# Kernel optimization log

Measured on AMD Instinct MI355X. Metric: run time of the kernel, lower is better.

The kernel has to match this reference:

```python
import jax, jax.numpy as jnp
import numpy as np
from jax import lax

B, N, S = 4, 16384, 4096
D1, D2 = 128, 256
MLP = (256, 128)
EPS_W = 1e-8
EPS_BN = 1e-5
BIG = 1e8


def setup_inputs() -> dict:
    key = jax.random.key(0)
    ks = jax.random.split(key, 10)
    inp = {
        "xyz1": jax.random.normal(ks[0], (B, 3, N), jnp.float32),
        "xyz2": jax.random.normal(ks[1], (B, 3, S), jnp.float32),
        "points1": jax.random.normal(ks[2], (B, D1, N), jnp.float32),
        "points2": jax.random.normal(ks[3], (B, D2, S), jnp.float32),
        "idx1": jnp.repeat(jnp.arange(B, dtype=jnp.int32), N).reshape(B, N),
        "idx2": jnp.repeat(jnp.arange(B, dtype=jnp.int32), S).reshape(B, S),
    }
    cin = D1 + D2
    inp["w1"] = jax.random.normal(ks[4], (MLP[0], cin), jnp.float32) * 0.05
    inp["b1"] = jnp.zeros((MLP[0],), jnp.float32)
    inp["g1"] = jnp.ones((MLP[0],), jnp.float32)
    inp["be1"] = jnp.zeros((MLP[0],), jnp.float32)
    inp["w2"] = jax.random.normal(ks[5], (MLP[1], MLP[0]), jnp.float32) * 0.05
    inp["b2"] = jnp.zeros((MLP[1],), jnp.float32)
    inp["g2"] = jnp.ones((MLP[1],), jnp.float32)
    inp["be2"] = jnp.zeros((MLP[1],), jnp.float32)
    return inp


def _bn_relu(x, gamma, beta):
    # training-mode batchnorm over (B, N) per channel, then relu; x: [B, C, N]
    mean = jnp.mean(x, axis=(0, 2), keepdims=True)
    var = jnp.var(x, axis=(0, 2), keepdims=True)  # biased, as torch BN
    xn = (x - mean) * lax.rsqrt(var + EPS_BN)
    return jax.nn.relu(xn * gamma[None, :, None] + beta[None, :, None])


def _fp_forward(xyz1, xyz2, points1, points2, idx1, idx2,
                w1, b1, g1, be1, w2, b2, g2, be2):
    x1 = jnp.transpose(xyz1, (0, 2, 1))  # [B, N, 3]
    x2 = jnp.transpose(xyz2, (0, 2, 1))  # [B, S, 3]
    p2 = jnp.transpose(points2, (0, 2, 1))  # [B, S, D2]

    # squared pairwise distances [B, N, S]
    d = -2.0 * jnp.einsum('bnc,bsc->bns', x1, x2)
    d = d + jnp.sum(x1 * x1, -1)[:, :, None] + jnp.sum(x2 * x2, -1)[:, None, :]
    d = jnp.where(idx1[:, :, None] == idx2[:, None, :], d, jnp.inf)

    # 3 nearest neighbors (top-k on negated distances == sort-ascending take 3)
    neg_d3, idx3 = lax.top_k(-d, 3)          # [B, N, 3]
    d3 = -neg_d3
    recip = 1.0 / (d3 + EPS_W)
    weight = recip / jnp.sum(recip, axis=2, keepdims=True)
    weight = jnp.where(d3 > BIG, 0.0, weight)
    weight = jnp.nan_to_num(weight)

    gathered = jax.vmap(lambda p, i: p[i])(p2, idx3)   # [B, N, 3, D2]
    interp = jnp.sum(gathered * weight[..., None], axis=2)  # [B, N, D2]

    newp = jnp.concatenate([jnp.transpose(points1, (0, 2, 1)), interp], axis=-1)
    newp = jnp.transpose(newp, (0, 2, 1))  # [B, D1+D2, N]

    # 1x1 conv -> BN -> relu, twice
    h = jnp.einsum('bcn,oc->bon', newp, w1) + b1[None, :, None]
    h = _bn_relu(h, g1, be1)
    h = jnp.einsum('bcn,oc->bon', h, w2) + b2[None, :, None]
    h = _bn_relu(h, g2, be2)
    return h


def reference(xyz1, xyz2, points1, points2, idx1, idx2,
              w1, b1, g1, be1, w2, b2, g2, be2):
    return _fp_forward(xyz1, xyz2, points1, points2, idx1, idx2,
                       w1, b1, g1, be1, w2, b2, g2, be2)
```

## Files before the change

kernel.cpp:

```cpp
#include <hip/hip_runtime.h>
#include <hip/hip_bf16.h>

#define INF_F (__builtin_inff())

typedef __attribute__((ext_vector_type(8))) short bf16x8;
typedef __attribute__((ext_vector_type(4))) float f32x4;

__device__ __forceinline__ unsigned short f2bf(float f) {
  __hip_bfloat16 h = __float2bfloat16(f);
  return __builtin_bit_cast(unsigned short, h);
}
__device__ __forceinline__ float bf2f(unsigned short u) {
  return __uint_as_float((unsigned)u << 16);
}


__global__ __launch_bounds__(256) void transpose_k(const float* __restrict__ in,
                                                   float* __restrict__ out) {
  __shared__ float tile[32][33];
  int b = blockIdx.z;
  int s0 = blockIdx.x * 32;
  int k0 = blockIdx.y * 32;
  int tx = threadIdx.x, ty = threadIdx.y;
  const float* src = in + ((size_t)b * 256 + k0) * 4096 + s0;
  for (int r = ty; r < 32; r += 8) tile[r][tx] = src[(size_t)r * 4096 + tx];
  __syncthreads();
  float* dst = out + ((size_t)b * 4096 + s0) * 256 + k0;
  for (int r = ty; r < 32; r += 8) dst[(size_t)r * 256 + tx] = tile[tx][r];
}

__global__ __launch_bounds__(256) void p1t_k(const float* __restrict__ p1,
                                             unsigned short* __restrict__ X) {
  __shared__ float tile[32][33];
  int b = blockIdx.z;
  int n0 = blockIdx.x * 32;
  int c0 = blockIdx.y * 32;
  int tx = threadIdx.x, ty = threadIdx.y;
  const float* src = p1 + ((size_t)b * 128 + c0) * 16384 + n0;
  for (int r = ty; r < 32; r += 8) tile[r][tx] = src[(size_t)r * 16384 + tx];
  __syncthreads();
  for (int r = ty; r < 32; r += 8)
    X[((size_t)(b * 16384 + n0 + r)) * 384 + c0 + tx] = f2bf(tile[tx][r]);
}

__global__ __launch_bounds__(256) void wcvt_k(const float* __restrict__ w1,
                                              const float* __restrict__ w2,
                                              unsigned short* __restrict__ w1b,
                                              unsigned short* __restrict__ w2b) {
  int id = blockIdx.x * 256 + threadIdx.x;
  if (id < 98304) w1b[id] = f2bf(w1[id]);
  else w2b[id - 98304] = f2bf(w2[id - 98304]);
}

__global__ __launch_bounds__(256) void knn_k(const float* __restrict__ xyz1,
                                             const float* __restrict__ xyz2,
                                             const int* __restrict__ idx1,
                                             const int* __restrict__ idx2,
                                             float* __restrict__ rec) {
  __shared__ float4 sP[2048];
  int bid = blockIdx.x;
  int nchunk = bid >> 1, shalf = bid & 1;
  int b = nchunk >> 7;
  int n0 = (nchunk & 127) * 128;
  int t = threadIdx.x;
  int q = t & 127, sp = t >> 7;
  int n = n0 + q;
  int common = idx1[b * 16384 + n0];
  int sbase = shalf << 11;
  for (int s = t; s < 2048; s += 256) {
    int gs = sbase + s;
    float x = xyz2[(b * 3 + 0) * 4096 + gs];
    float y = xyz2[(b * 3 + 1) * 4096 + gs];
    float z = xyz2[(b * 3 + 2) * 4096 + gs];
    float w = fmaf(x, x, fmaf(y, y, z * z));
    int sid = idx2[b * 4096 + gs];
    w = (sid == common) ? w : 3e38f;
    sP[s] = make_float4(x, y, z, w);
  }
  __syncthreads();
  float px = xyz1[(b * 3 + 0) * 16384 + n];
  float py = xyz1[(b * 3 + 1) * 16384 + n];
  float pz = xyz1[(b * 3 + 2) * 16384 + n];
  int myid = idx1[b * 16384 + n];
  float pn = fmaf(px, px, fmaf(py, py, pz * pz));
  float e0 = INF_F, e1 = INF_F, e2 = INF_F;
  int j0 = 0, j1 = 0, j2 = 0;
  int sBeg = sp << 10, sEnd = sBeg + 1024;
#pragma unroll 4
  for (int s = sBeg; s < sEnd; ++s) {
    float4 p = sP[s];
    float dot = fmaf(px, p.x, fmaf(py, p.y, pz * p.z));
    float d = fmaf(-2.f, dot, pn + p.w);
    if (d < e2) {
      int sj = sbase + s;
      bool l0 = d < e0, l1 = d < e1;
      e2 = l1 ? e1 : d;
      j2 = l1 ? j1 : sj;
      e1 = l0 ? e0 : (l1 ? d : e1);
      j1 = l0 ? j0 : (l1 ? sj : j1);
      e0 = l0 ? d : e0;
      j0 = l0 ? sj : j0;
    }
  }
  if (__builtin_expect(myid != common, 0)) {
    e0 = e1 = e2 = INF_F; j0 = j1 = j2 = 0;
    for (int s = sBeg; s < sEnd; ++s) {
      int gs = sbase + s;
      float x = xyz2[(b * 3 + 0) * 4096 + gs];
      float y = xyz2[(b * 3 + 1) * 4096 + gs];
      float z = xyz2[(b * 3 + 2) * 4096 + gs];
      float w = fmaf(x, x, fmaf(y, y, z * z));
      float dot = fmaf(px, x, fmaf(py, y, pz * z));
      float d = fmaf(-2.f, dot, pn + w);
      d = (idx2[b * 4096 + gs] == myid) ? d : INF_F;
      if (d < e2) {
        bool l0 = d < e0, l1 = d < e1;
        e2 = l1 ? e1 : d; j2 = l1 ? j1 : gs;
        e1 = l0 ? e0 : (l1 ? d : e1); j1 = l0 ? j0 : (l1 ? gs : j1);
        e0 = l0 ? d : e0; j0 = l0 ? gs : j0;
      }
    }
  }
  __syncthreads();
  float* sf = (float*)sP;
  int* si = (int*)sP;
  if (sp == 1) {
    sf[0 * 128 + q] = e0; sf[1 * 128 + q] = e1; sf[2 * 128 + q] = e2;
    si[3 * 128 + q] = j0; si[4 * 128 + q] = j1; si[5 * 128 + q] = j2;
  }
  __syncthreads();
  if (t < 128) {
#pragma unroll
    for (int w = 0; w < 3; ++w) {
      float d = sf[w * 128 + t];
      int sj = si[(w + 3) * 128 + t];
      bool l0 = (d < e0) || (d == e0 && sj < j0);
      bool l1 = (d < e1) || (d == e1 && sj < j1);
      bool l2 = (d < e2) || (d == e2 && sj < j2);
      e2 = l1 ? e1 : (l2 ? d : e2);
      j2 = l1 ? j1 : (l2 ? sj : j2);
      e1 = l0 ? e0 : (l1 ? d : e1);
      j1 = l0 ? j0 : (l1 ? sj : j1);
      e0 = l0 ? d : e0;
      j0 = l0 ? sj : j0;
    }
    float* r = &rec[(((size_t)nchunk * 128 + t) * 2 + shalf) * 6];
    r[0] = e0; r[1] = e1; r[2] = e2;
    ((int*)r)[3] = j0; ((int*)r)[4] = j1; ((int*)r)[5] = j2;
  }
}

__global__ __launch_bounds__(256) void knnmerge_k(const float* __restrict__ rec,
                                                  int* __restrict__ idx3,
                                                  float* __restrict__ wgt) {
  int i = blockIdx.x * 256 + threadIdx.x;
  const float* rA = &rec[(size_t)i * 12];
  const int* iA = (const int*)rA;
  float e0 = rA[0], e1 = rA[1], e2 = rA[2];
  int j0 = iA[3], j1 = iA[4], j2 = iA[5];
#pragma unroll
  for (int w = 0; w < 3; ++w) {
    float d = rA[6 + w];
    int sj = iA[9 + w];
    bool l0 = (d < e0) || (d == e0 && sj < j0);
    bool l1 = (d < e1) || (d == e1 && sj < j1);
    bool l2 = (d < e2) || (d == e2 && sj < j2);
    e2 = l1 ? e1 : (l2 ? d : e2);
    j2 = l1 ? j1 : (l2 ? sj : j2);
    e1 = l0 ? e0 : (l1 ? d : e1);
    j1 = l0 ? j0 : (l1 ? sj : j1);
    e0 = l0 ? d : e0;
    j0 = l0 ? sj : j0;
  }
  float r0 = 1.f / (e0 + 1e-8f);
  float r1 = 1.f / (e1 + 1e-8f);
  float r2 = 1.f / (e2 + 1e-8f);
  float rs = r0 + r1 + r2;
  float w0 = (e0 > 1e8f) ? 0.f : r0 / rs;
  float w1 = (e1 > 1e8f) ? 0.f : r1 / rs;
  float w2 = (e2 > 1e8f) ? 0.f : r2 / rs;
  idx3[(size_t)i * 3 + 0] = j0; idx3[(size_t)i * 3 + 1] = j1; idx3[(size_t)i * 3 + 2] = j2;
  wgt[(size_t)i * 3 + 0] = w0;  wgt[(size_t)i * 3 + 1] = w1;  wgt[(size_t)i * 3 + 2] = w2;
}

__global__ __launch_bounds__(256) void interp_k(const float* __restrict__ p2t,
                                                const int* __restrict__ idx3,
                                                const float* __restrict__ wgt,
                                                unsigned short* __restrict__ X) {
  int i0 = blockIdx.x * 128;
  int b = i0 >> 14;
  int k = threadIdx.x;
  const float* base = p2t + (size_t)b * 4096 * 256;
#pragma unroll 2
  for (int ii = 0; ii < 128; ++ii) {
    int i = i0 + ii;
    int id0 = idx3[i * 3 + 0], id1 = idx3[i * 3 + 1], id2 = idx3[i * 3 + 2];
    float w0 = wgt[i * 3 + 0], w1v = wgt[i * 3 + 1], w2v = wgt[i * 3 + 2];
    float v = w0 * base[id0 * 256 + k];
    v = fmaf(w1v, base[id1 * 256 + k], v);
    v = fmaf(w2v, base[id2 * 256 + k], v);
    X[(size_t)i * 384 + 128 + k] = f2bf(v);
  }
}

__global__ __launch_bounds__(256) void gemm1_k(const unsigned short* __restrict__ X,
                                               const unsigned short* __restrict__ Wb,
                                               unsigned short* __restrict__ h1T) {
  __shared__ unsigned short sW[128][40];
  __shared__ unsigned short sX[128][40];
  int t = threadIdx.x;
  int i0 = blockIdx.x * 128;
  int c0 = blockIdx.y * 128;
  int w = t >> 6, lane = t & 63;
  int wc = (w & 1) * 64, wn = (w >> 1) * 64;
  int l15 = lane & 15, g = lane >> 4;
  f32x4 acc[4][4];
#pragma unroll
  for (int a = 0; a < 4; ++a)
#pragma unroll
    for (int bq = 0; bq < 4; ++bq) acc[a][bq] = (f32x4)0.f;
  int sr = t & 127, sh = t >> 7;
  for (int kc = 0; kc < 12; ++kc) {
    int k0 = kc * 32;
    __syncthreads();
    {
      const uint4* gw = (const uint4*)&Wb[(size_t)(c0 + sr) * 384 + k0 + sh * 16];
      uint4 v0 = gw[0], v1 = gw[1];
      *(uint4*)&sW[sr][sh * 16] = v0;
      *(uint4*)&sW[sr][sh * 16 + 8] = v1;
      const uint4* gx = (const uint4*)&X[(size_t)(i0 + sr) * 384 + k0 + sh * 16];
      uint4 x0 = gx[0], x1 = gx[1];
      *(uint4*)&sX[sr][sh * 16] = x0;
      *(uint4*)&sX[sr][sh * 16 + 8] = x1;
    }
    __syncthreads();
    bf16x8 a[4], b[4];
#pragma unroll
    for (int tm = 0; tm < 4; ++tm)
      a[tm] = *(const bf16x8*)&sW[wc + tm * 16 + l15][g * 8];
#pragma unroll
    for (int tn = 0; tn < 4; ++tn)
      b[tn] = *(const bf16x8*)&sX[wn + tn * 16 + l15][g * 8];
#pragma unroll
    for (int tm = 0; tm < 4; ++tm)
#pragma unroll
      for (int tn = 0; tn < 4; ++tn)
        acc[tm][tn] = __builtin_amdgcn_mfma_f32_16x16x32_bf16(a[tm], b[tn], acc[tm][tn], 0, 0, 0);
  }
#pragma unroll
  for (int tm = 0; tm < 4; ++tm)
#pragma unroll
    for (int tn = 0; tn < 4; ++tn) {
      int c = c0 + wc + tm * 16 + g * 4;
      int n = i0 + wn + tn * 16 + l15;
      f32x4 v = acc[tm][tn];
      ushort4 o;
      o.x = f2bf(v[0]); o.y = f2bf(v[1]); o.z = f2bf(v[2]); o.w = f2bf(v[3]);
      *(ushort4*)&h1T[(size_t)n * 256 + c] = o;
    }
}

__global__ __launch_bounds__(256) void bnstats1_k(const unsigned short* __restrict__ h,
                                                  float* __restrict__ part) {
  int t = threadIdx.x, q = t & 63, ro = t >> 6;
  int r0 = blockIdx.x * 256;
  float s0 = 0, s1 = 0, s2 = 0, s3 = 0, q0 = 0, q1 = 0, q2 = 0, q3 = 0;
  for (int it = 0; it < 64; ++it) {
    size_t r = r0 + it * 4 + ro;
    ushort4 v = *(const ushort4*)&h[r * 256 + q * 4];
    float f0 = bf2f(v.x), f1 = bf2f(v.y), f2 = bf2f(v.z), f3 = bf2f(v.w);
    s0 += f0; q0 += f0 * f0;
    s1 += f1; q1 += f1 * f1;
    s2 += f2; q2 += f2 * f2;
    s3 += f3; q3 += f3 * f3;
  }
  __shared__ float sm[256][8];
  sm[t][0] = s0; sm[t][1] = s1; sm[t][2] = s2; sm[t][3] = s3;
  sm[t][4] = q0; sm[t][5] = q1; sm[t][6] = q2; sm[t][7] = q3;
  __syncthreads();
  if (t < 64) {
#pragma unroll
    for (int j = 1; j < 4; ++j)
#pragma unroll
      for (int e = 0; e < 8; ++e) sm[t][e] += sm[t + 64 * j][e];
#pragma unroll
    for (int i = 0; i < 4; ++i) {
      part[((size_t)blockIdx.x * 256 + t * 4 + i) * 2 + 0] = sm[t][i];
      part[((size_t)blockIdx.x * 256 + t * 4 + i) * 2 + 1] = sm[t][4 + i];
    }
  }
}

__global__ __launch_bounds__(256) void bnstats2_k(const float* __restrict__ o2,
                                                  float* __restrict__ part) {
  int t = threadIdx.x, q = t & 31, ro = t >> 5;
  int r0 = blockIdx.x * 256;
  float s0 = 0, s1 = 0, s2 = 0, s3 = 0, q0 = 0, q1 = 0, q2 = 0, q3 = 0;
  for (int it = 0; it < 32; ++it) {
    size_t r = r0 + it * 8 + ro;
    float4 v = *(const float4*)&o2[r * 128 + q * 4];
    s0 += v.x; q0 += v.x * v.x;
    s1 += v.y; q1 += v.y * v.y;
    s2 += v.z; q2 += v.z * v.z;
    s3 += v.w; q3 += v.w * v.w;
  }
  __shared__ float sm[256][8];
  sm[t][0] = s0; sm[t][1] = s1; sm[t][2] = s2; sm[t][3] = s3;
  sm[t][4] = q0; sm[t][5] = q1; sm[t][6] = q2; sm[t][7] = q3;
  __syncthreads();
  if (t < 32) {
#pragma unroll
    for (int j = 1; j < 8; ++j)
#pragma unroll
      for (int e = 0; e < 8; ++e) sm[t][e] += sm[t + 32 * j][e];
#pragma unroll
    for (int i = 0; i < 4; ++i) {
      part[((size_t)blockIdx.x * 128 + t * 4 + i) * 2 + 0] = sm[t][i];
      part[((size_t)blockIdx.x * 128 + t * 4 + i) * 2 + 1] = sm[t][4 + i];
    }
  }
}

template <int C>
__global__ __launch_bounds__(256) void bnfold_k(const float* __restrict__ part,
                                                const float* __restrict__ g,
                                                const float* __restrict__ be,
                                                float* __restrict__ A,
                                                float* __restrict__ Cc) {
  int c = threadIdx.x;
  if (c >= C) return;
  float s1 = 0.f, s2 = 0.f;
  for (int b = 0; b < 256; ++b) {
    s1 += part[((size_t)b * C + c) * 2 + 0];
    s2 += part[((size_t)b * C + c) * 2 + 1];
  }
  float mean = s1 * (1.f / 65536.f);
  float var = s2 * (1.f / 65536.f) - mean * mean;
  float a = g[c] * rsqrtf(var + 1e-5f);
  A[c] = a;
  Cc[c] = be[c] - mean * a;
}

__global__ __launch_bounds__(256) void bnapply1_k(const unsigned short* __restrict__ h,
                                                  const float* __restrict__ A,
                                                  const float* __restrict__ C,
                                                  unsigned short* __restrict__ o) {
  size_t idx = ((size_t)blockIdx.x * 256 + threadIdx.x) * 8;
  int c = (int)(idx & 255);
  uint4 v = *(const uint4*)&h[idx];
  float4 a0 = *(const float4*)&A[c], a1 = *(const float4*)&A[c + 4];
  float4 c0 = *(const float4*)&C[c], c1 = *(const float4*)&C[c + 4];
  unsigned r[4] = {v.x, v.y, v.z, v.w};
  float av[8] = {a0.x, a0.y, a0.z, a0.w, a1.x, a1.y, a1.z, a1.w};
  float cv[8] = {c0.x, c0.y, c0.z, c0.w, c1.x, c1.y, c1.z, c1.w};
  unsigned w[4];
#pragma unroll
  for (int e = 0; e < 4; ++e) {
    float f0 = bf2f((unsigned short)(r[e] & 0xFFFFu));
    float f1 = bf2f((unsigned short)(r[e] >> 16));
    f0 = fmaxf(fmaf(av[2 * e], f0, cv[2 * e]), 0.f);
    f1 = fmaxf(fmaf(av[2 * e + 1], f1, cv[2 * e + 1]), 0.f);
    w[e] = (unsigned)f2bf(f0) | ((unsigned)f2bf(f1) << 16);
  }
  uint4 ov = {w[0], w[1], w[2], w[3]};
  *(uint4*)&o[idx] = ov;
}

__global__ __launch_bounds__(256) void gemm2_k(const unsigned short* __restrict__ Xb,
                                               const unsigned short* __restrict__ Wb,
                                               float* __restrict__ o2) {
  __shared__ unsigned short sW[128][40];
  __shared__ unsigned short sX[128][40];
  int t = threadIdx.x;
  int i0 = blockIdx.x * 128;
  int w = t >> 6, lane = t & 63;
  int wc = (w & 1) * 64, wn = (w >> 1) * 64;
  int l15 = lane & 15, g = lane >> 4;
  f32x4 acc[4][4];
#pragma unroll
  for (int a = 0; a < 4; ++a)
#pragma unroll
    for (int bq = 0; bq < 4; ++bq) acc[a][bq] = (f32x4)0.f;
  int sr = t & 127, sh = t >> 7;
  for (int kc = 0; kc < 8; ++kc) {
    int k0 = kc * 32;
    __syncthreads();
    {
      const uint4* gw = (const uint4*)&Wb[(size_t)sr * 256 + k0 + sh * 16];
      uint4 v0 = gw[0], v1 = gw[1];
      *(uint4*)&sW[sr][sh * 16] = v0;
      *(uint4*)&sW[sr][sh * 16 + 8] = v1;
      const uint4* gx = (const uint4*)&Xb[(size_t)(i0 + sr) * 256 + k0 + sh * 16];
      uint4 x0 = gx[0], x1 = gx[1];
      *(uint4*)&sX[sr][sh * 16] = x0;
      *(uint4*)&sX[sr][sh * 16 + 8] = x1;
    }
    __syncthreads();
    bf16x8 a[4], b[4];
#pragma unroll
    for (int tm = 0; tm < 4; ++tm)
      a[tm] = *(const bf16x8*)&sW[wc + tm * 16 + l15][g * 8];
#pragma unroll
    for (int tn = 0; tn < 4; ++tn)
      b[tn] = *(const bf16x8*)&sX[wn + tn * 16 + l15][g * 8];
#pragma unroll
    for (int tm = 0; tm < 4; ++tm)
#pragma unroll
      for (int tn = 0; tn < 4; ++tn)
        acc[tm][tn] = __builtin_amdgcn_mfma_f32_16x16x32_bf16(a[tm], b[tn], acc[tm][tn], 0, 0, 0);
  }
#pragma unroll
  for (int tm = 0; tm < 4; ++tm)
#pragma unroll
    for (int tn = 0; tn < 4; ++tn) {
      int c = wc + tm * 16 + g * 4;
      int n = i0 + wn + tn * 16 + l15;
      f32x4 v = acc[tm][tn];
      *(float4*)&o2[(size_t)n * 128 + c] = make_float4(v[0], v[1], v[2], v[3]);
    }
}

__global__ __launch_bounds__(256) void final_k(const float* __restrict__ o2,
                                               const float* __restrict__ A,
                                               const float* __restrict__ C,
                                               float* __restrict__ out) {
  __shared__ float tile[32][33];
  int b = blockIdx.z;
  int n0 = blockIdx.x * 32;
  int c0 = blockIdx.y * 32;
  int tx = threadIdx.x, ty = threadIdx.y;
  float a = A[c0 + tx], cc = C[c0 + tx];
  for (int r = ty; r < 32; r += 8) {
    float v = o2[(size_t)(b * 16384 + n0 + r) * 128 + c0 + tx];
    tile[r][tx] = fmaxf(fmaf(a, v, cc), 0.f);
  }
  __syncthreads();
  for (int r = ty; r < 32; r += 8)
    out[((size_t)(b * 128 + c0 + r)) * 16384 + n0 + tx] = tile[tx][r];
}

extern "C" void kernel_launch(void* const* d_in, const int* in_sizes, int n_in,
                              void* d_out, int out_size, void* d_ws, size_t ws_size,
                              hipStream_t stream) {
  const float* xyz1 = (const float*)d_in[0];
  const float* xyz2 = (const float*)d_in[1];
  const float* p1   = (const float*)d_in[2];
  const float* p2   = (const float*)d_in[3];
  const int*   idx1 = (const int*)d_in[4];
  const int*   idx2 = (const int*)d_in[5];
  const float* w1   = (const float*)d_in[6];
  const float* g1   = (const float*)d_in[8];
  const float* be1  = (const float*)d_in[9];
  const float* w2   = (const float*)d_in[10];
  const float* g2   = (const float*)d_in[12];
  const float* be2  = (const float*)d_in[13];
  float* out = (float*)d_out;

  char* ws = (char*)d_ws;
  int*            idx3 = (int*)(ws + 0x0);
  float*          wgt  = (float*)(ws + 0xC0000);
  float*          rec  = (float*)(ws + 0x180000);
  unsigned short* X    = (unsigned short*)(ws + 0x480000);
  unsigned short* h1bn = (unsigned short*)(ws + 0x480000);
  unsigned short* h1T  = (unsigned short*)(ws + 0x3480000);
  float*          p2t  = (float*)(ws + 0x3480000);
  float*          o2   = (float*)(ws + 0x5480000);
  unsigned short* w1b  = (unsigned short*)(ws + 0x7480000);
  unsigned short* w2b  = (unsigned short*)(ws + 0x74B0000);
  float*          part1 = (float*)(ws + 0x74C0000);
  float*          part2 = (float*)(ws + 0x7540000);
  float*          a1   = (float*)(ws + 0x7580000);
  float*          c1   = a1 + 256;
  float*          a2   = c1 + 256;
  float*          c2   = a2 + 128;

  hipLaunchKernelGGL(transpose_k, dim3(128, 8, 4), dim3(32, 8), 0, stream, p2, p2t);
  hipLaunchKernelGGL(wcvt_k, dim3(512), dim3(256), 0, stream, w1, w2, w1b, w2b);
  hipLaunchKernelGGL(p1t_k, dim3(512, 4, 4), dim3(32, 8), 0, stream, p1, X);
  hipLaunchKernelGGL(knn_k, dim3(1024), dim3(256), 0, stream,
                     xyz1, xyz2, idx1, idx2, rec);
  hipLaunchKernelGGL(knnmerge_k, dim3(256), dim3(256), 0, stream, rec, idx3, wgt);
  hipLaunchKernelGGL(interp_k, dim3(512), dim3(256), 0, stream, p2t, idx3, wgt, X);
  hipLaunchKernelGGL(gemm1_k, dim3(512, 2), dim3(256), 0, stream, X, w1b, h1T);
  hipLaunchKernelGGL(bnstats1_k, dim3(256), dim3(256), 0, stream, h1T, part1);
  hipLaunchKernelGGL((bnfold_k<256>), dim3(1), dim3(256), 0, stream, part1, g1, be1, a1, c1);
  hipLaunchKernelGGL(bnapply1_k, dim3(8192), dim3(256), 0, stream, h1T, a1, c1, h1bn);
  hipLaunchKernelGGL(gemm2_k, dim3(512), dim3(256), 0, stream, h1bn, w2b, o2);
  hipLaunchKernelGGL(bnstats2_k, dim3(256), dim3(256), 0, stream, o2, part2);
  hipLaunchKernelGGL((bnfold_k<128>), dim3(1), dim3(256), 0, stream, part2, g2, be2, a2, c2);
  hipLaunchKernelGGL(final_k, dim3(512, 4, 4), dim3(32, 8), 0, stream, o2, a2, c2, out);
}
```

Baseline: 262.1 us.

## Fold BN1 apply into gemm2 loads and restructure KNN into 4-way S split

```diff
diff --git a/kernel.cpp b/kernel.cpp
--- a/kernel.cpp
+++ b/kernel.cpp
@@ -57,17 +57,15 @@
                                              const int* __restrict__ idx1,
                                              const int* __restrict__ idx2,
                                              float* __restrict__ rec) {
-  __shared__ float4 sP[2048];
+  __shared__ float4 sP[1024];
   int bid = blockIdx.x;
-  int nchunk = bid >> 1, shalf = bid & 1;
-  int b = nchunk >> 7;
-  int n0 = (nchunk & 127) * 128;
+  int nchunk = bid >> 2, sq = bid & 3;
+  int b = nchunk >> 5;
+  int n0 = (nchunk & 31) * 512;
   int t = threadIdx.x;
-  int q = t & 127, sp = t >> 7;
-  int n = n0 + q;
   int common = idx1[b * 16384 + n0];
-  int sbase = shalf << 11;
-  for (int s = t; s < 2048; s += 256) {
+  int sbase = sq << 10;
+  for (int s = t; s < 1024; s += 256) {
     int gs = sbase + s;
     float x = xyz2[(b * 3 + 0) * 4096 + gs];
     float y = xyz2[(b * 3 + 1) * 4096 + gs];
@@ -78,62 +76,104 @@
     sP[s] = make_float4(x, y, z, w);
   }
   __syncthreads();
-  float px = xyz1[(b * 3 + 0) * 16384 + n];
-  float py = xyz1[(b * 3 + 1) * 16384 + n];
-  float pz = xyz1[(b * 3 + 2) * 16384 + n];
-  int myid = idx1[b * 16384 + n];
-  float pn = fmaf(px, px, fmaf(py, py, pz * pz));
-  float e0 = INF_F, e1 = INF_F, e2 = INF_F;
-  int j0 = 0, j1 = 0, j2 = 0;
-  int sBeg = sp << 10, sEnd = sBeg + 1024;
+  int nla = n0 + t, nlb = n0 + 256 + t;
+  float pxa = xyz1[(b * 3 + 0) * 16384 + nla];
+  float pya = xyz1[(b * 3 + 1) * 16384 + nla];
+  float pza = xyz1[(b * 3 + 2) * 16384 + nla];
+  float pxb = xyz1[(b * 3 + 0) * 16384 + nlb];
+  float pyb = xyz1[(b * 3 + 1) * 16384 + nlb];
+  float pzb = xyz1[(b * 3 + 2) * 16384 + nlb];
+  int ida = idx1[b * 16384 + nla];
+  int idb = idx1[b * 16384 + nlb];
+  float pna = fmaf(pxa, pxa, fmaf(pya, pya, pza * pza));
+  float pnb = fmaf(pxb, pxb, fmaf(pyb, pyb, pzb * pzb));
+  float e0a = INF_F, e1a = INF_F, e2a = INF_F;
+  float e0b = INF_F, e1b = INF_F, e2b = INF_F;
+  int j0a = 0, j1a = 0, j2a = 0, j0b = 0, j1b = 0, j2b = 0;
 #pragma unroll 4
-  for (int s = sBeg; s < sEnd; ++s) {
+  for (int s = 0; s < 1024; ++s) {
     float4 p = sP[s];
-    float dot = fmaf(px, p.x, fmaf(py, p.y, pz * p.z));
-    float d = fmaf(-2.f, dot, pn + p.w);
-    if (d < e2) {
+    float dota = fmaf(pxa, p.x, fmaf(pya, p.y, pza * p.z));
+    float da = fmaf(-2.f, dota, pna + p.w);
+    float dotb = fmaf(pxb, p.x, fmaf(pyb, p.y, pzb * p.z));
+    float db = fmaf(-2.f, dotb, pnb + p.w);
+    if (da < e2a) {
       int sj = sbase + s;
-      bool l0 = d < e0, l1 = d < e1;
-      e2 = l1 ? e1 : d;
-      j2 = l1 ? j1 : sj;
-      e1 = l0 ? e0 : (l1 ? d : e1);
-      j1 = l0 ? j0 : (l1 ? sj : j1);
-      e0 = l0 ? d : e0;
-      j0 = l0 ? sj : j0;
-    }
-  }
-  if (__builtin_expect(myid != common, 0)) {
-    e0 = e1 = e2 = INF_F; j0 = j1 = j2 = 0;
-    for (int s = sBeg; s < sEnd; ++s) {
+      bool l0 = da < e0a, l1 = da < e1a;
+      e2a = l1 ? e1a : da;           j2a = l1 ? j1a : sj;
+      e1a = l0 ? e0a : (l1 ? da : e1a); j1a = l0 ? j0a : (l1 ? sj : j1a);
+      e0a = l0 ? da : e0a;           j0a = l0 ? sj : j0a;
+    }
+    if (db < e2b) {
+      int sj = sbase + s;
+      bool l0 = db < e0b, l1 = db < e1b;
+      e2b = l1 ? e1b : db;           j2b = l1 ? j1b : sj;
+      e1b = l0 ? e0b : (l1 ? db : e1b); j1b = l0 ? j0b : (l1 ? sj : j1b);
+      e0b = l0 ? db : e0b;           j0b = l0 ? sj : j0b;
+    }
+  }
+  if (__builtin_expect(ida != common, 0)) {
+    e0a = e1a = e2a = INF_F; j0a = j1a = j2a = 0;
+    for (int s = 0; s < 1024; ++s) {
       int gs = sbase + s;
       float x = xyz2[(b * 3 + 0) * 4096 + gs];
       float y = xyz2[(b * 3 + 1) * 4096 + gs];
       float z = xyz2[(b * 3 + 2) * 4096 + gs];
       float w = fmaf(x, x, fmaf(y, y, z * z));
-      float dot = fmaf(px, x, fmaf(py, y, pz * z));
-      float d = fmaf(-2.f, dot, pn + w);
-      d = (idx2[b * 4096 + gs] == myid) ? d : INF_F;
-      if (d < e2) {
-        bool l0 = d < e0, l1 = d < e1;
-        e2 = l1 ? e1 : d; j2 = l1 ? j1 : gs;
-        e1 = l0 ? e0 : (l1 ? d : e1); j1 = l0 ? j0 : (l1 ? gs : j1);
-        e0 = l0 ? d : e0; j0 = l0 ? gs : j0;
+      float d = fmaf(-2.f, fmaf(pxa, x, fmaf(pya, y, pza * z)), pna + w);
+      d = (idx2[b * 4096 + gs] == ida) ? d : INF_F;
+      if (d < e2a) {
+        bool l0 = d < e0a, l1 = d < e1a;
+        e2a = l1 ? e1a : d; j2a = l1 ? j1a : gs;
+        e1a = l0 ? e0a : (l1 ? d : e1a); j1a = l0 ? j0a : (l1 ? gs : j1a);
+        e0a = l0 ? d : e0a; j0a = l0 ? gs : j0a;
       }
     }
   }
-  __syncthreads();
-  float* sf = (float*)sP;
-  int* si = (int*)sP;
-  if (sp == 1) {
-    sf[0 * 128 + q] = e0; sf[1 * 128 + q] = e1; sf[2 * 128 + q] = e2;
-    si[3 * 128 + q] = j0; si[4 * 128 + q] = j1; si[5 * 128 + q] = j2;
-  }
-  __syncthreads();
-  if (t < 128) {
+  if (__builtin_expect(idb != common, 0)) {
+    e0b = e1b = e2b = INF_F; j0b = j1b = j2b = 0;
+    for (int s = 0; s < 1024; ++s) {
+      int gs = sbase + s;
+      float x = xyz2[(b * 3 + 0) * 4096 + gs];
+      float y = xyz2[(b * 3 + 1) * 4096 + gs];
+      float z = xyz2[(b * 3 + 2) * 4096 + gs];
+      float w = fmaf(x, x, fmaf(y, y, z * z));
+      float d = fmaf(-2.f, fmaf(pxb, x, fmaf(pyb, y, pzb * z)), pnb + w);
+      d = (idx2[b * 4096 + gs] == idb) ? d : INF_F;
+      if (d < e2b) {
+        bool l0 = d < e0b, l1 = d < e1b;
+        e2b = l1 ? e1b : d; j2b = l1 ? j1b : gs;
+        e1b = l0 ? e0b : (l1 ? d : e1b); j1b = l0 ? j0b : (l1 ? gs : j1b);
+        e0b = l0 ? d : e0b; j0b = l0 ? gs : j0b;
+      }
+    }
+  }
+  {
+    float* r = &rec[(((size_t)(b * 16384 + nla)) * 4 + sq) * 6];
+    r[0] = e0a; r[1] = e1a; r[2] = e2a;
+    ((int*)r)[3] = j0a; ((int*)r)[4] = j1a; ((int*)r)[5] = j2a;
+  }
+  {
+    float* r = &rec[(((size_t)(b * 16384 + nlb)) * 4 + sq) * 6];
+    r[0] = e0b; r[1] = e1b; r[2] = e2b;
+    ((int*)r)[3] = j0b; ((int*)r)[4] = j1b; ((int*)r)[5] = j2b;
+  }
+}
+
+__global__ __launch_bounds__(256) void knnmerge_k(const float* __restrict__ rec,
+                                                  int* __restrict__ idx3,
+                                                  float* __restrict__ wgt) {
+  int i = blockIdx.x * 256 + threadIdx.x;
+  const float* rA = &rec[(size_t)i * 24];
+  const int* iA = (const int*)rA;
+  float e0 = rA[0], e1 = rA[1], e2 = rA[2];
+  int j0 = iA[3], j1 = iA[4], j2 = iA[5];
+#pragma unroll
+  for (int c = 1; c < 4; ++c) {
 #pragma unroll
     for (int w = 0; w < 3; ++w) {
-      float d = sf[w * 128 + t];
-      int sj = si[(w + 3) * 128 + t];
+      float d = rA[c * 6 + w];
+      int sj = iA[c * 6 + 3 + w];
       bool l0 = (d < e0) || (d == e0 && sj < j0);
       bool l1 = (d < e1) || (d == e1 && sj < j1);
       bool l2 = (d < e2) || (d == e2 && sj < j2);
@@ -144,33 +184,6 @@
       e0 = l0 ? d : e0;
       j0 = l0 ? sj : j0;
     }
-    float* r = &rec[(((size_t)nchunk * 128 + t) * 2 + shalf) * 6];
-    r[0] = e0; r[1] = e1; r[2] = e2;
-    ((int*)r)[3] = j0; ((int*)r)[4] = j1; ((int*)r)[5] = j2;
-  }
-}
-
-__global__ __launch_bounds__(256) void knnmerge_k(const float* __restrict__ rec,
-                                                  int* __restrict__ idx3,
-                                                  float* __restrict__ wgt) {
-  int i = blockIdx.x * 256 + threadIdx.x;
-  const float* rA = &rec[(size_t)i * 12];
-  const int* iA = (const int*)rA;
-  float e0 = rA[0], e1 = rA[1], e2 = rA[2];
-  int j0 = iA[3], j1 = iA[4], j2 = iA[5];
-#pragma unroll
-  for (int w = 0; w < 3; ++w) {
-    float d = rA[6 + w];
-    int sj = iA[9 + w];
-    bool l0 = (d < e0) || (d == e0 && sj < j0);
-    bool l1 = (d < e1) || (d == e1 && sj < j1);
-    bool l2 = (d < e2) || (d == e2 && sj < j2);
-    e2 = l1 ? e1 : (l2 ? d : e2);
-    j2 = l1 ? j1 : (l2 ? sj : j2);
-    e1 = l0 ? e0 : (l1 ? d : e1);
-    j1 = l0 ? j0 : (l1 ? sj : j1);
-    e0 = l0 ? d : e0;
-    j0 = l0 ? sj : j0;
   }
   float r0 = 1.f / (e0 + 1e-8f);
   float r1 = 1.f / (e1 + 1e-8f);
@@ -341,33 +354,10 @@
   Cc[c] = be[c] - mean * a;
 }
 
-__global__ __launch_bounds__(256) void bnapply1_k(const unsigned short* __restrict__ h,
-                                                  const float* __restrict__ A,
-                                                  const float* __restrict__ C,
-                                                  unsigned short* __restrict__ o) {
-  size_t idx = ((size_t)blockIdx.x * 256 + threadIdx.x) * 8;
-  int c = (int)(idx & 255);
-  uint4 v = *(const uint4*)&h[idx];
-  float4 a0 = *(const float4*)&A[c], a1 = *(const float4*)&A[c + 4];
-  float4 c0 = *(const float4*)&C[c], c1 = *(const float4*)&C[c + 4];
-  unsigned r[4] = {v.x, v.y, v.z, v.w};
-  float av[8] = {a0.x, a0.y, a0.z, a0.w, a1.x, a1.y, a1.z, a1.w};
-  float cv[8] = {c0.x, c0.y, c0.z, c0.w, c1.x, c1.y, c1.z, c1.w};
-  unsigned w[4];
-#pragma unroll
-  for (int e = 0; e < 4; ++e) {
-    float f0 = bf2f((unsigned short)(r[e] & 0xFFFFu));
-    float f1 = bf2f((unsigned short)(r[e] >> 16));
-    f0 = fmaxf(fmaf(av[2 * e], f0, cv[2 * e]), 0.f);
-    f1 = fmaxf(fmaf(av[2 * e + 1], f1, cv[2 * e + 1]), 0.f);
-    w[e] = (unsigned)f2bf(f0) | ((unsigned)f2bf(f1) << 16);
-  }
-  uint4 ov = {w[0], w[1], w[2], w[3]};
-  *(uint4*)&o[idx] = ov;
-}
-
-__global__ __launch_bounds__(256) void gemm2_k(const unsigned short* __restrict__ Xb,
+__global__ __launch_bounds__(256) void gemm2_k(const unsigned short* __restrict__ h1T,
                                                const unsigned short* __restrict__ Wb,
+                                               const float* __restrict__ A,
+                                               const float* __restrict__ C,
                                                float* __restrict__ o2) {
   __shared__ unsigned short sW[128][40];
   __shared__ unsigned short sX[128][40];
@@ -384,16 +374,30 @@
   int sr = t & 127, sh = t >> 7;
   for (int kc = 0; kc < 8; ++kc) {
     int k0 = kc * 32;
+    int kcol = k0 + sh * 16;
     __syncthreads();
     {
-      const uint4* gw = (const uint4*)&Wb[(size_t)sr * 256 + k0 + sh * 16];
+      const uint4* gw = (const uint4*)&Wb[(size_t)sr * 256 + kcol];
       uint4 v0 = gw[0], v1 = gw[1];
       *(uint4*)&sW[sr][sh * 16] = v0;
       *(uint4*)&sW[sr][sh * 16 + 8] = v1;
-      const uint4* gx = (const uint4*)&Xb[(size_t)(i0 + sr) * 256 + k0 + sh * 16];
+      const uint4* gx = (const uint4*)&h1T[(size_t)(i0 + sr) * 256 + kcol];
       uint4 x0 = gx[0], x1 = gx[1];
-      *(uint4*)&sX[sr][sh * 16] = x0;
-      *(uint4*)&sX[sr][sh * 16 + 8] = x1;
+      unsigned rr[8] = {x0.x, x0.y, x0.z, x0.w, x1.x, x1.y, x1.z, x1.w};
+      unsigned ww[8];
+#pragma unroll
+      for (int e = 0; e < 8; ++e) {
+        int ch = kcol + 2 * e;
+        float f0 = bf2f((unsigned short)(rr[e] & 0xFFFFu));
+        float f1 = bf2f((unsigned short)(rr[e] >> 16));
+        f0 = fmaxf(fmaf(A[ch], f0, C[ch]), 0.f);
+        f1 = fmaxf(fmaf(A[ch + 1], f1, C[ch + 1]), 0.f);
+        ww[e] = (unsigned)f2bf(f0) | ((unsigned)f2bf(f1) << 16);
+      }
+      uint4 y0 = {ww[0], ww[1], ww[2], ww[3]};
+      uint4 y1 = {ww[4], ww[5], ww[6], ww[7]};
+      *(uint4*)&sX[sr][sh * 16] = y0;
+      *(uint4*)&sX[sr][sh * 16 + 8] = y1;
     }
     __syncthreads();
     bf16x8 a[4], b[4];
@@ -460,16 +464,15 @@
   int*            idx3 = (int*)(ws + 0x0);
   float*          wgt  = (float*)(ws + 0xC0000);
   float*          rec  = (float*)(ws + 0x180000);
-  unsigned short* X    = (unsigned short*)(ws + 0x480000);
-  unsigned short* h1bn = (unsigned short*)(ws + 0x480000);
-  unsigned short* h1T  = (unsigned short*)(ws + 0x3480000);
-  float*          p2t  = (float*)(ws + 0x3480000);
-  float*          o2   = (float*)(ws + 0x5480000);
-  unsigned short* w1b  = (unsigned short*)(ws + 0x7480000);
-  unsigned short* w2b  = (unsigned short*)(ws + 0x74B0000);
-  float*          part1 = (float*)(ws + 0x74C0000);
-  float*          part2 = (float*)(ws + 0x7540000);
-  float*          a1   = (float*)(ws + 0x7580000);
+  unsigned short* X    = (unsigned short*)(ws + 0x780000);
+  unsigned short* h1T  = (unsigned short*)(ws + 0x3780000);
+  float*          p2t  = (float*)(ws + 0x3780000);
+  float*          o2   = (float*)(ws + 0x5780000);
+  unsigned short* w1b  = (unsigned short*)(ws + 0x7780000);
+  unsigned short* w2b  = (unsigned short*)(ws + 0x77B0000);
+  float*          part1 = (float*)(ws + 0x77C0000);
+  float*          part2 = (float*)(ws + 0x7840000);
+  float*          a1   = (float*)(ws + 0x7880000);
   float*          c1   = a1 + 256;
   float*          a2   = c1 + 256;
   float*          c2   = a2 + 128;
@@ -477,15 +480,14 @@
   hipLaunchKernelGGL(transpose_k, dim3(128, 8, 4), dim3(32, 8), 0, stream, p2, p2t);
   hipLaunchKernelGGL(wcvt_k, dim3(512), dim3(256), 0, stream, w1, w2, w1b, w2b);
   hipLaunchKernelGGL(p1t_k, dim3(512, 4, 4), dim3(32, 8), 0, stream, p1, X);
-  hipLaunchKernelGGL(knn_k, dim3(1024), dim3(256), 0, stream,
+  hipLaunchKernelGGL(knn_k, dim3(512), dim3(256), 0, stream,
                      xyz1, xyz2, idx1, idx2, rec);
   hipLaunchKernelGGL(knnmerge_k, dim3(256), dim3(256), 0, stream, rec, idx3, wgt);
   hipLaunchKernelGGL(interp_k, dim3(512), dim3(256), 0, stream, p2t, idx3, wgt, X);
   hipLaunchKernelGGL(gemm1_k, dim3(512, 2), dim3(256), 0, stream, X, w1b, h1T);
   hipLaunchKernelGGL(bnstats1_k, dim3(256), dim3(256), 0, stream, h1T, part1);
   hipLaunchKernelGGL((bnfold_k<256>), dim3(1), dim3(256), 0, stream, part1, g1, be1, a1, c1);
-  hipLaunchKernelGGL(bnapply1_k, dim3(8192), dim3(256), 0, stream, h1T, a1, c1, h1bn);
-  hipLaunchKernelGGL(gemm2_k, dim3(512), dim3(256), 0, stream, h1bn, w2b, o2);
+  hipLaunchKernelGGL(gemm2_k, dim3(512), dim3(256), 0, stream, h1T, w2b, a1, c1, o2);
   hipLaunchKernelGGL(bnstats2_k, dim3(256), dim3(256), 0, stream, o2, part2);
   hipLaunchKernelGGL((bnfold_k<128>), dim3(1), dim3(256), 0, stream, part2, g2, be2, a2, c2);
   hipLaunchKernelGGL(final_k, dim3(512, 4, 4), dim3(32, 8), 0, stream, o2, a2, c2, out);
```

Result: slower. 296.9 us (+13.2%).
